# Performance work log

Hardware: AMD Instinct MI355X
Metric: run time of the kernel (lower is better)

Reference implementation:

```python
import jax, jax.numpy as jnp
import numpy as np

N_NODES = 100000
N_EDGES = 1600000
D_IN = 128
D_OUT = 128


def setup_inputs() -> dict:
    key = jax.random.key(0)
    k1, k2, k3, k4 = jax.random.split(key, 4)
    feat = jax.random.normal(k1, (N_NODES, D_IN), dtype=jnp.float32)
    weight = jax.random.normal(k2, (D_IN, D_OUT), dtype=jnp.float32) * (1.0 / np.sqrt(D_IN))
    src = jax.random.randint(k3, (N_EDGES,), 0, N_NODES, dtype=jnp.int64)
    dst = jax.random.randint(k4, (N_EDGES,), 0, N_NODES, dtype=jnp.int64)
    return {"feat": feat, "weight": weight, "src": src, "dst": dst}


def reference(feat, weight, src, dst):
    n = feat.shape[0]
    ones = jnp.ones(src.shape[0], dtype=feat.dtype)
    # norm == 'both': scale source features by out_degree^{-1/2}
    out_deg = jnp.clip(jax.ops.segment_sum(ones, src, num_segments=n), 1.0)
    feat_src = feat * (out_deg ** -0.5)[:, None]  # [N, D_in]
    # update_all(copy_src, sum): gather src features, segment-sum into dst
    agg = jax.ops.segment_sum(feat_src[src], dst, num_segments=n)  # [N, D_in]
    # dense transform with external weight
    rst = agg @ weight  # [N, D_out]
    # destination-side normalization by in_degree^{-1/2}
    in_deg = jnp.clip(jax.ops.segment_sum(ones, dst, num_segments=n), 1.0)
    rst = rst * (in_deg ** -0.5)[:, None]
    return rst
```

## Files before the change

### kernel.cpp

```cpp
#include <hip/hip_runtime.h>
#include <stdint.h>


#define DIM 128
#define BK 64
#define MAXB 2048
#define CAPB 1280
#define SK 128
#define MAXS 1024
#define CAPS 2560
#define PT 512
#define EPT 13
#define CHUNK (PT * EPT)

typedef unsigned int uint;
typedef unsigned short ushortT;
typedef __attribute__((ext_vector_type(8))) _Float16 f16x8;
typedef __attribute__((ext_vector_type(4))) float f32x4;

__device__ __forceinline__ ushortT f2bf(float x) {
    uint u = __float_as_uint(x);
    u = (u + 0x7FFFu + ((u >> 16) & 1u)) >> 16;
    return (ushortT)u;
}
__device__ __forceinline__ float bflo(uint u) { return __uint_as_float(u << 16); }
__device__ __forceinline__ float bfhi(uint u) { return __uint_as_float(u & 0xffff0000u); }

union H16 { _Float16 h; ushortT u; };
__device__ __forceinline__ ushortT f2h_bits(float x) {
    H16 t; t.h = (_Float16)x; return t.u;
}

__global__ __launch_bounds__(PT) void part(
    const int* __restrict__ src, const int* __restrict__ dst,
    int* __restrict__ curB, int* __restrict__ curS,
    int* __restrict__ pairs, unsigned char* __restrict__ srcb,
    int E, int NPB, int NPS) {
    __shared__ int cD[MAXB], lofD[MAXB], gbD[MAXB];
    __shared__ int cS[MAXS], lofS[MAXS], gbS[MAXS];
    __shared__ int bufD[CHUNK];
    __shared__ unsigned char bufS[CHUNK];
    __shared__ int wtotD[8], wtotS[8];

    int tid = threadIdx.x;
    long long base = (long long)blockIdx.x * CHUNK;
    for (int i = tid; i < MAXB; i += PT) cD[i] = 0;
    for (int i = tid; i < MAXS; i += PT) cS[i] = 0;
    __syncthreads();

    int sv[EPT], dv[EPT], lrD[EPT], lrS[EPT];
#pragma unroll
    for (int j = 0; j < EPT; ++j) {
        long long e = base + tid + j * PT;
        bool ok = e < E;
        int s = 0, d = 0;
        if (ok) { s = src[e]; d = dst[e]; }
        sv[j] = s; dv[j] = d;
        lrD[j] = ok ? atomicAdd(&cD[d >> 6], 1) : 0;
        lrS[j] = ok ? atomicAdd(&cS[s >> 7], 1) : 0;
    }
    __syncthreads();

    {
        int lane = tid & 63, wv = tid >> 6;
        int b0 = tid << 2;
        int s0 = cD[b0], s1 = cD[b0 + 1], s2 = cD[b0 + 2], s3 = cD[b0 + 3];
        int tsum = s0 + s1 + s2 + s3;
        int incl = tsum;
        for (int o = 1; o < 64; o <<= 1) {
            int y = __shfl_up(incl, o, 64);
            if (lane >= o) incl += y;
        }
        if (lane == 63) wtotD[wv] = incl;

        int a0idx = tid << 1;
        int t0 = cS[a0idx], t1 = cS[a0idx + 1];
        int ssum = t0 + t1;
        int sincl = ssum;
        for (int o = 1; o < 64; o <<= 1) {
            int y = __shfl_up(sincl, o, 64);
            if (lane >= o) sincl += y;
        }
        if (lane == 63) wtotS[wv] = sincl;
        __syncthreads();

        int wbD = 0, wbS = 0;
        for (int x = 0; x < wv; ++x) { wbD += wtotD[x]; wbS += wtotS[x]; }
        int exD = wbD + incl - tsum;
        lofD[b0] = exD;
        lofD[b0 + 1] = exD + s0;
        lofD[b0 + 2] = exD + s0 + s1;
        lofD[b0 + 3] = exD + s0 + s1 + s2;
        int exS = wbS + sincl - ssum;
        lofS[a0idx] = exS;
        lofS[a0idx + 1] = exS + t0;
    }
    __syncthreads();

    for (int i = tid; i < NPB; i += PT) {
        int c = cD[i];
        gbD[i] = c ? atomicAdd(&curB[i], c) : 0;
    }
    for (int i = tid; i < NPS; i += PT) {
        int c = cS[i];
        gbS[i] = c ? atomicAdd(&curS[i], c) : 0;
    }

#pragma unroll
    for (int j = 0; j < EPT; ++j) {
        long long e = base + tid + j * PT;
        if (e < E) {
            bufD[lofD[dv[j] >> 6] + lrD[j]] = (sv[j] << 6) | (dv[j] & 63);
            bufS[lofS[sv[j] >> 7] + lrS[j]] = (unsigned char)(sv[j] & 127);
        }
    }
    __syncthreads();

    int cntE = (int)(((long long)E - base < (long long)CHUNK) ? (E - base) : CHUNK);
    for (int i = tid; i < cntE; i += PT) {
        int lo = 0, hi = NPB - 1;
        while (lo < hi) { int mid = (lo + hi + 1) >> 1; if (lofD[mid] <= i) lo = mid; else hi = mid - 1; }
        int pos = gbD[lo] + (i - lofD[lo]);
        if (pos < CAPB) pairs[(size_t)lo * CAPB + pos] = bufD[i];
    }
    for (int i = tid; i < cntE; i += PT) {
        int lo = 0, hi = NPS - 1;
        while (lo < hi) { int mid = (lo + hi + 1) >> 1; if (lofS[mid] <= i) lo = mid; else hi = mid - 1; }
        int pos = gbS[lo] + (i - lofS[lo]);
        if (pos < CAPS) srcb[(size_t)lo * CAPS + pos] = bufS[i];
    }
}

__global__ __launch_bounds__(256) void deg(
    const int* __restrict__ curS, const unsigned char* __restrict__ srcb,
    float* __restrict__ oscale, int N) {
    __shared__ int hist[SK];
    int p = blockIdx.x, tid = threadIdx.x;
    if (tid < SK) hist[tid] = 0;
    __syncthreads();
    int cnt = min(curS[p], CAPS);
    const unsigned char* b = &srcb[(size_t)p * CAPS];
    for (int i = tid; i < cnt; i += 256) atomicAdd(&hist[b[i]], 1);
    __syncthreads();
    if (tid < SK) {
        int node = p * SK + tid;
        if (node < N) oscale[node] = rsqrtf((float)max(hist[tid], 1));
    }
}

__global__ __launch_bounds__(256) void wtr(const float* __restrict__ W,
                                           ushortT* __restrict__ Bt) {
    __shared__ float Ws[32][132];
    int tid = threadIdx.x;
    int k0 = blockIdx.x * 32;
    for (int i = tid; i < 1024; i += 256) {
        int r = i >> 5, cc = (i & 31) << 2;
        *(float4*)&Ws[r][cc] = *(const float4*)&W[(size_t)(k0 + r) * DIM + cc];
    }
    __syncthreads();
    int n = tid >> 1, ks = (tid & 1) << 4;
    uint o[8];
#pragma unroll
    for (int j = 0; j < 8; ++j) {
        ushortT a = f2h_bits(Ws[ks + 2 * j][n]);
        ushortT b = f2h_bits(Ws[ks + 2 * j + 1][n]);
        o[j] = (uint)a | ((uint)b << 16);
    }
    ushortT* bp = &Bt[(size_t)n * DIM + k0 + ks];
    *(uint4*)bp = *(uint4*)&o[0];
    *(uint4*)(bp + 8) = *(uint4*)&o[4];
}

__global__ __launch_bounds__(256) void gemm_h(
    const float* __restrict__ feat, const ushortT* __restrict__ Bt,
    const float* __restrict__ oscale, ushortT* __restrict__ h, int M) {
    __shared__ __align__(16) ushortT Bs[128 * 128];

    int tid = threadIdx.x;
    for (int i = tid; i < 2048; i += 256) {
        int n = i >> 4, s = i & 15;
        uint4 v = ((const uint4*)Bt)[i];
        *(uint4*)&Bs[n * 128 + ((s << 3) ^ ((n & 7) << 3))] = v;
    }

    int wid = tid >> 6;
    int l = tid & 63;
    int lr = l & 15;
    int lk = l >> 4;
    int m0 = blockIdx.x * 64;
    int row = m0 + wid * 16 + lr;
    bool ok = row < M;
    int rr = ok ? row : 0;
    float sc = ok ? oscale[rr] : 0.f;
    const float* fp = feat + (size_t)rr * DIM;

    f32x4 acc[8];
    f32x4 z = {0.f, 0.f, 0.f, 0.f};
#pragma unroll
    for (int n = 0; n < 8; ++n) acc[n] = z;

    __syncthreads();

#pragma unroll
    for (int kc = 0; kc < 4; ++kc) {
        int kb = kc * 32 + lk * 8;
        float4 x0 = *(const float4*)&fp[kb];
        float4 x1 = *(const float4*)&fp[kb + 4];
        float f[8] = {x0.x * sc, x0.y * sc, x0.z * sc, x0.w * sc,
                      x1.x * sc, x1.y * sc, x1.z * sc, x1.w * sc};
        f16x8 ah, al;
#pragma unroll
        for (int j = 0; j < 8; ++j) {
            _Float16 hi = (_Float16)f[j];
            ah[j] = hi;
            al[j] = (_Float16)(f[j] - (float)hi);
        }
#pragma unroll
        for (int n = 0; n < 8; ++n) {
            int brow = n * 16 + lr;
            int bidx = brow * 128 + (kb ^ ((brow & 7) << 3));
            f16x8 b = *(const f16x8*)&Bs[bidx];
            acc[n] = __builtin_amdgcn_mfma_f32_16x16x32_f16(ah, b, acc[n], 0, 0, 0);
            acc[n] = __builtin_amdgcn_mfma_f32_16x16x32_f16(al, b, acc[n], 0, 0, 0);
        }
    }

#pragma unroll
    for (int r = 0; r < 4; ++r) {
        int ro = m0 + wid * 16 + lk * 4 + r;
        if (ro < M) {
            uint w0 = (uint)f2bf(acc[0][r]) | ((uint)f2bf(acc[1][r]) << 16);
            uint w1 = (uint)f2bf(acc[2][r]) | ((uint)f2bf(acc[3][r]) << 16);
            uint w2 = (uint)f2bf(acc[4][r]) | ((uint)f2bf(acc[5][r]) << 16);
            uint w3 = (uint)f2bf(acc[6][r]) | ((uint)f2bf(acc[7][r]) << 16);
            uint4 o = make_uint4(w0, w1, w2, w3);
            *(uint4*)&h[(size_t)ro * DIM + (lr << 3)] = o;
        }
    }
}

__global__ __launch_bounds__(512) void aggp(
    const ushortT* __restrict__ h, const int* __restrict__ pairs,
    const int* __restrict__ curB, float* __restrict__ out, int N) {
    __shared__ int raw[CAPB];
    __shared__ int sorted[CAPB];
    __shared__ int hist[64], offs[64], cur[64];
    int p = blockIdx.x;
    int tid = threadIdx.x;
    if (tid < 64) hist[tid] = 0;
    __syncthreads();
    int cnt = min(curB[p], CAPB);
    const int* pb = &pairs[(size_t)p * CAPB];
    for (int i = tid; i < cnt; i += 512) {
        int w = pb[i];
        raw[i] = w;
        atomicAdd(&hist[w & 63], 1);
    }
    __syncthreads();
    if (tid < 64) {
        int x = hist[tid], incl = x;
        for (int o = 1; o < 64; o <<= 1) {
            int y = __shfl_up(incl, o, 64);
            if (tid >= o) incl += y;
        }
        offs[tid] = incl - x;
        cur[tid] = incl - x;
    }
    __syncthreads();
    for (int i = tid; i < cnt; i += 512) {
        int w = raw[i];
        int slot = atomicAdd(&cur[w & 63], 1);
        sorted[slot] = w >> 6;
    }
    __syncthreads();
    int g = tid >> 4, c = tid & 15;
    int cb = c << 3;
    for (int nd = g; nd < 64; nd += 32) {
        int node = p * BK + nd;
        if (node >= N) continue;
        int start = offs[nd];
        int degn = hist[nd];
        int end = min(start + degn, CAPB);
        float a0 = 0.f, a1 = 0.f, a2 = 0.f, a3 = 0.f;
        float a4 = 0.f, a5 = 0.f, a6 = 0.f, a7 = 0.f;
        int e = start;
        for (; e + 8 <= end; e += 8) {
            int s0 = sorted[e],     s1 = sorted[e + 1];
            int s2 = sorted[e + 2], s3 = sorted[e + 3];
            int s4 = sorted[e + 4], s5 = sorted[e + 5];
            int s6 = sorted[e + 6], s7 = sorted[e + 7];
            uint4 v0 = *(const uint4*)&h[(size_t)s0 * DIM + cb];
            uint4 v1 = *(const uint4*)&h[(size_t)s1 * DIM + cb];
            uint4 v2 = *(const uint4*)&h[(size_t)s2 * DIM + cb];
            uint4 v3 = *(const uint4*)&h[(size_t)s3 * DIM + cb];
            uint4 v4 = *(const uint4*)&h[(size_t)s4 * DIM + cb];
            uint4 v5 = *(const uint4*)&h[(size_t)s5 * DIM + cb];
            uint4 v6 = *(const uint4*)&h[(size_t)s6 * DIM + cb];
            uint4 v7 = *(const uint4*)&h[(size_t)s7 * DIM + cb];
            a0 += ((bflo(v0.x) + bflo(v1.x)) + (bflo(v2.x) + bflo(v3.x))) +
                  ((bflo(v4.x) + bflo(v5.x)) + (bflo(v6.x) + bflo(v7.x)));
            a1 += ((bfhi(v0.x) + bfhi(v1.x)) + (bfhi(v2.x) + bfhi(v3.x))) +
                  ((bfhi(v4.x) + bfhi(v5.x)) + (bfhi(v6.x) + bfhi(v7.x)));
            a2 += ((bflo(v0.y) + bflo(v1.y)) + (bflo(v2.y) + bflo(v3.y))) +
                  ((bflo(v4.y) + bflo(v5.y)) + (bflo(v6.y) + bflo(v7.y)));
            a3 += ((bfhi(v0.y) + bfhi(v1.y)) + (bfhi(v2.y) + bfhi(v3.y))) +
                  ((bfhi(v4.y) + bfhi(v5.y)) + (bfhi(v6.y) + bfhi(v7.y)));
            a4 += ((bflo(v0.z) + bflo(v1.z)) + (bflo(v2.z) + bflo(v3.z))) +
                  ((bflo(v4.z) + bflo(v5.z)) + (bflo(v6.z) + bflo(v7.z)));
            a5 += ((bfhi(v0.z) + bfhi(v1.z)) + (bfhi(v2.z) + bfhi(v3.z))) +
                  ((bfhi(v4.z) + bfhi(v5.z)) + (bfhi(v6.z) + bfhi(v7.z)));
            a6 += ((bflo(v0.w) + bflo(v1.w)) + (bflo(v2.w) + bflo(v3.w))) +
                  ((bflo(v4.w) + bflo(v5.w)) + (bflo(v6.w) + bflo(v7.w)));
            a7 += ((bfhi(v0.w) + bfhi(v1.w)) + (bfhi(v2.w) + bfhi(v3.w))) +
                  ((bfhi(v4.w) + bfhi(v5.w)) + (bfhi(v6.w) + bfhi(v7.w)));
        }
        for (; e < end; ++e) {
            uint4 v = *(const uint4*)&h[(size_t)sorted[e] * DIM + cb];
            a0 += bflo(v.x); a1 += bfhi(v.x);
            a2 += bflo(v.y); a3 += bfhi(v.y);
            a4 += bflo(v.z); a5 += bfhi(v.z);
            a6 += bflo(v.w); a7 += bfhi(v.w);
        }
        float scn = rsqrtf((float)max(degn, 1));
        size_t ob = (size_t)node * DIM + c;
        out[ob]       = a0 * scn;
        out[ob + 16]  = a1 * scn;
        out[ob + 32]  = a2 * scn;
        out[ob + 48]  = a3 * scn;
        out[ob + 64]  = a4 * scn;
        out[ob + 80]  = a5 * scn;
        out[ob + 96]  = a6 * scn;
        out[ob + 112] = a7 * scn;
    }
}

extern "C" void kernel_launch(void* const* d_in, const int* in_sizes, int n_in,
                              void* d_out, int out_size, void* d_ws, size_t ws_size,
                              hipStream_t stream) {
    const float* feat = (const float*)d_in[0];
    const float* W    = (const float*)d_in[1];
    const int*   src  = (const int*)d_in[2];
    const int*   dst  = (const int*)d_in[3];
    float* out = (float*)d_out;

    int N = in_sizes[0] / DIM;
    int E = in_sizes[2];
    int NPB = (N + BK - 1) / BK;
    int NPS = (N + SK - 1) / SK;

    int* curB = (int*)d_ws;
    int* curS = curB + NPB;
    float* oscale = (float*)(curS + NPS);
    int* pairs = (int*)(oscale + N);
    unsigned char* srcb = (unsigned char*)(pairs + (size_t)NPB * CAPB);
    uintptr_t bp = (uintptr_t)(srcb + (size_t)NPS * CAPS);
    ushortT* Bt = (ushortT*)((bp + 15) & ~(uintptr_t)15);
    ushortT* h = Bt + DIM * DIM;

    hipMemsetAsync(curB, 0, (size_t)(NPB + NPS) * sizeof(int), stream);

    int nb = (E + CHUNK - 1) / CHUNK;
    wtr<<<4, 256, 0, stream>>>(W, Bt);
    part<<<nb, PT, 0, stream>>>(src, dst, curB, curS, pairs, srcb, E, NPB, NPS);
    deg<<<NPS, 256, 0, stream>>>(curS, srcb, oscale, N);
    gemm_h<<<(N + 63) / 64, 256, 0, stream>>>(feat, Bt, oscale, h, N);
    aggp<<<NPB, 512, 0, stream>>>(h, pairs, curB, out, N);
}
```

Before: 242.9 us.

## Fuse weight transpose and degree histogram into GEMM; cache bucket IDs in partition

The partition kernel now stores each edge's destination bucket id in shared memory during the local scatter, so the global write loop no longer runs a binary search per edge for the dst buckets. The separate weight-transpose and out-degree kernels are removed. Each GEMM block converts W to fp16 in its own LDS and builds the out-degree histogram for its 128-node slice directly. This cuts two launches and the round trip through global memory for oscale and Bt. In exchange, every GEMM block re-reads the full W, and each histogram is rebuilt by two blocks.

```diff
diff --git a/kernel.cpp b/kernel.cpp
--- a/kernel.cpp
+++ b/kernel.cpp
@@ -36,9 +36,10 @@
     int* __restrict__ curB, int* __restrict__ curS,
     int* __restrict__ pairs, unsigned char* __restrict__ srcb,
     int E, int NPB, int NPS) {
-    __shared__ int cD[MAXB], lofD[MAXB], gbD[MAXB];
-    __shared__ int cS[MAXS], lofS[MAXS], gbS[MAXS];
+    __shared__ int cD[MAXB], lofD[MAXB];
+    __shared__ int cS[MAXS], lofS[MAXS];
     __shared__ int bufD[CHUNK];
+    __shared__ ushortT bufB[CHUNK];
     __shared__ unsigned char bufS[CHUNK];
     __shared__ int wtotD[8], wtotS[8];
 
@@ -99,18 +100,21 @@
 
     for (int i = tid; i < NPB; i += PT) {
         int c = cD[i];
-        gbD[i] = c ? atomicAdd(&curB[i], c) : 0;
+        cD[i] = c ? atomicAdd(&curB[i], c) : 0;
     }
     for (int i = tid; i < NPS; i += PT) {
         int c = cS[i];
-        gbS[i] = c ? atomicAdd(&curS[i], c) : 0;
+        cS[i] = c ? atomicAdd(&curS[i], c) : 0;
     }
 
 #pragma unroll
     for (int j = 0; j < EPT; ++j) {
         long long e = base + tid + j * PT;
         if (e < E) {
-            bufD[lofD[dv[j] >> 6] + lrD[j]] = (sv[j] << 6) | (dv[j] & 63);
+            int b = dv[j] >> 6;
+            int pos = lofD[b] + lrD[j];
+            bufD[pos] = (sv[j] << 6) | (dv[j] & 63);
+            bufB[pos] = (ushortT)b;
             bufS[lofS[sv[j] >> 7] + lrS[j]] = (unsigned char)(sv[j] & 127);
         }
     }
@@ -118,70 +122,57 @@
 
     int cntE = (int)(((long long)E - base < (long long)CHUNK) ? (E - base) : CHUNK);
     for (int i = tid; i < cntE; i += PT) {
-        int lo = 0, hi = NPB - 1;
-        while (lo < hi) { int mid = (lo + hi + 1) >> 1; if (lofD[mid] <= i) lo = mid; else hi = mid - 1; }
-        int pos = gbD[lo] + (i - lofD[lo]);
-        if (pos < CAPB) pairs[(size_t)lo * CAPB + pos] = bufD[i];
+        int b = bufB[i];
+        int pos = cD[b] + (i - lofD[b]);
+        if (pos < CAPB) pairs[(size_t)b * CAPB + pos] = bufD[i];
     }
     for (int i = tid; i < cntE; i += PT) {
         int lo = 0, hi = NPS - 1;
         while (lo < hi) { int mid = (lo + hi + 1) >> 1; if (lofS[mid] <= i) lo = mid; else hi = mid - 1; }
-        int pos = gbS[lo] + (i - lofS[lo]);
+        int pos = cS[lo] + (i - lofS[lo]);
         if (pos < CAPS) srcb[(size_t)lo * CAPS + pos] = bufS[i];
     }
 }
 
-__global__ __launch_bounds__(256) void deg(
+__global__ __launch_bounds__(256) void gemm_h(
+    const float* __restrict__ feat, const float* __restrict__ W,
     const int* __restrict__ curS, const unsigned char* __restrict__ srcb,
-    float* __restrict__ oscale, int N) {
+    ushortT* __restrict__ h, int M) {
+    __shared__ __align__(16) ushortT Bs[128 * 128];
     __shared__ int hist[SK];
-    int p = blockIdx.x, tid = threadIdx.x;
+
+    int tid = threadIdx.x;
     if (tid < SK) hist[tid] = 0;
-    __syncthreads();
-    int cnt = min(curS[p], CAPS);
-    const unsigned char* b = &srcb[(size_t)p * CAPS];
-    for (int i = tid; i < cnt; i += 256) atomicAdd(&hist[b[i]], 1);
-    __syncthreads();
-    if (tid < SK) {
-        int node = p * SK + tid;
-        if (node < N) oscale[node] = rsqrtf((float)max(hist[tid], 1));
-    }
-}
-
-__global__ __launch_bounds__(256) void wtr(const float* __restrict__ W,
-                                           ushortT* __restrict__ Bt) {
-    __shared__ float Ws[32][132];
-    int tid = threadIdx.x;
-    int k0 = blockIdx.x * 32;
-    for (int i = tid; i < 1024; i += 256) {
-        int r = i >> 5, cc = (i & 31) << 2;
-        *(float4*)&Ws[r][cc] = *(const float4*)&W[(size_t)(k0 + r) * DIM + cc];
-    }
-    __syncthreads();
-    int n = tid >> 1, ks = (tid & 1) << 4;
-    uint o[8];
-#pragma unroll
-    for (int j = 0; j < 8; ++j) {
-        ushortT a = f2h_bits(Ws[ks + 2 * j][n]);
-        ushortT b = f2h_bits(Ws[ks + 2 * j + 1][n]);
-        o[j] = (uint)a | ((uint)b << 16);
-    }
-    ushortT* bp = &Bt[(size_t)n * DIM + k0 + ks];
-    *(uint4*)bp = *(uint4*)&o[0];
-    *(uint4*)(bp + 8) = *(uint4*)&o[4];
-}
-
-__global__ __launch_bounds__(256) void gemm_h(
-    const float* __restrict__ feat, const ushortT* __restrict__ Bt,
-    const float* __restrict__ oscale, ushortT* __restrict__ h, int M) {
-    __shared__ __align__(16) ushortT Bs[128 * 128];
-
-    int tid = threadIdx.x;
-    for (int i = tid; i < 2048; i += 256) {
-        int n = i >> 4, s = i & 15;
-        uint4 v = ((const uint4*)Bt)[i];
-        *(uint4*)&Bs[n * 128 + ((s << 3) ^ ((n & 7) << 3))] = v;
-    }
+
+    {
+        int kk = (tid >> 2) << 1;
+        int n0 = (tid & 3) << 5;
+        const float* w0 = &W[(size_t)kk * DIM + n0];
+        const float* w1 = w0 + DIM;
+#pragma unroll
+        for (int jj = 0; jj < 8; ++jj) {
+            float4 a = *(const float4*)&w0[jj * 4];
+            float4 b = *(const float4*)&w1[jj * 4];
+            float av[4] = {a.x, a.y, a.z, a.w};
+            float bv[4] = {b.x, b.y, b.z, b.w};
+#pragma unroll
+            for (int t = 0; t < 4; ++t) {
+                int n = n0 + jj * 4 + t;
+                uint u = (uint)f2h_bits(av[t]) | ((uint)f2h_bits(bv[t]) << 16);
+                int idx = n * 128 + (((kk >> 3) ^ (n & 7)) << 3) + (kk & 7);
+                *(uint*)&Bs[idx] = u;
+            }
+        }
+    }
+    __syncthreads();
+
+    int p = blockIdx.x >> 1;
+    {
+        int cnt = min(curS[p], CAPS);
+        const unsigned char* b = &srcb[(size_t)p * CAPS];
+        for (int i = tid; i < cnt; i += 256) atomicAdd(&hist[b[i]], 1);
+    }
+    __syncthreads();
 
     int wid = tid >> 6;
     int l = tid & 63;
@@ -191,15 +182,13 @@
     int row = m0 + wid * 16 + lr;
     bool ok = row < M;
     int rr = ok ? row : 0;
-    float sc = ok ? oscale[rr] : 0.f;
+    float sc = ok ? rsqrtf((float)max(hist[row & 127], 1)) : 0.f;
     const float* fp = feat + (size_t)rr * DIM;
 
     f32x4 acc[8];
     f32x4 z = {0.f, 0.f, 0.f, 0.f};
 #pragma unroll
     for (int n = 0; n < 8; ++n) acc[n] = z;
-
-    __syncthreads();
 
 #pragma unroll
     for (int kc = 0; kc < 4; ++kc) {
@@ -350,19 +339,15 @@
 
     int* curB = (int*)d_ws;
     int* curS = curB + NPB;
-    float* oscale = (float*)(curS + NPS);
-    int* pairs = (int*)(oscale + N);
+    int* pairs = curS + NPS;
     unsigned char* srcb = (unsigned char*)(pairs + (size_t)NPB * CAPB);
-    uintptr_t bp = (uintptr_t)(srcb + (size_t)NPS * CAPS);
-    ushortT* Bt = (ushortT*)((bp + 15) & ~(uintptr_t)15);
-    ushortT* h = Bt + DIM * DIM;
+    uintptr_t hp = (uintptr_t)(srcb + (size_t)NPS * CAPS);
+    ushortT* h = (ushortT*)((hp + 15) & ~(uintptr_t)15);
 
     hipMemsetAsync(curB, 0, (size_t)(NPB + NPS) * sizeof(int), stream);
 
     int nb = (E + CHUNK - 1) / CHUNK;
-    wtr<<<4, 256, 0, stream>>>(W, Bt);
     part<<<nb, PT, 0, stream>>>(src, dst, curB, curS, pairs, srcb, E, NPB, NPS);
-    deg<<<NPS, 256, 0, stream>>>(curS, srcb, oscale, N);
-    gemm_h<<<(N + 63) / 64, 256, 0, stream>>>(feat, Bt, oscale, h, N);
+    gemm_h<<<(N + 63) / 64, 256, 0, stream>>>(feat, W, curS, srcb, h, N);
     aggp<<<NPB, 512, 0, stream>>>(h, pairs, curB, out, N);
 }
```

Result: no change. 245.8 us (+1.2%).
